# Kernel tuning notes

Measured on AMD Instinct MI355X. Metric: run time of the kernel, lower is better.

Reference implementation:

```python
import jax, jax.numpy as jnp
import numpy as np

EPS = 1e-5

def hard_sigmoid(x):
    return jnp.clip(0.2 * x + 0.5, 0.0, 1.0)

def ln(x, g, b):
    m = jnp.mean(x, axis=-1, keepdims=True)
    std = jnp.sqrt(jnp.var(x, axis=-1, keepdims=True) + EPS)
    return g * ((x - m) / (std + EPS)) + b

def setup_inputs() -> dict:
    key = jax.random.key(0)
    k0, k1, k2 = jax.random.split(key, 3)
    B, T, I, H = 128, 128, 512, 512
    D = I + H
    x = jax.random.normal(k0, (B, T, I), dtype=jnp.float32)
    mask = jnp.ones((B, T), dtype=jnp.int32)
    W = jax.random.normal(k1, (D, H + 1), dtype=jnp.float32) * 0.02
    U = jax.random.normal(k2, (D, H + 1), dtype=jnp.float32) * 0.02
    b = jnp.zeros((H + 1,), dtype=jnp.float32)
    gammas = jnp.ones((2, H + 1), dtype=jnp.float32)
    betas = jnp.zeros((2, H + 1), dtype=jnp.float32)
    return {"x": x, "mask": mask, "W": W, "U": U, "b": b,
            "gammas": gammas, "betas": betas,
            "bucket_size": 128, "depth": 4, "input_dim": 512}

def reference(x, mask, W, U, b, gammas, betas, bucket_size, depth, input_dim):
    B, T, I = x.shape
    H = W.shape[1] - 1
    D = I + H
    # pad input to (input_dim | hidden_dim) layout, time-major, truncate to bucket
    xp = jnp.concatenate([x, jnp.zeros((B, T, H), x.dtype)], axis=-1)
    xs = jnp.transpose(xp, (1, 0, 2))[:bucket_size]          # (Tb, B, D)
    m = (mask.T[:bucket_size] > 0)                            # (Tb, B) bool
    first = jnp.zeros((1, B), dtype=bool)
    shift = jnp.concatenate([m[1:], first], axis=0)
    m2 = m & (~shift)
    m2 = jnp.concatenate([first, m2[:-1]], axis=0)            # (Tb, B)
    Tb = xs.shape[0]
    g0, g1 = gammas[0], gammas[1]
    b0, b1 = betas[0], betas[1]

    def hstep(carry, inp):
        h_tm1, fk_tm1, hv_tm1 = carry
        x_t, fkp_tm1, fkp, mk, mk2, hvp = inp
        sum2 = ln(h_tm1 @ U, g1, b1)                          # (B, H+1)
        s = ln(x_t @ W, g0, b0) + sum2 + b                    # (B, H+1)
        fk_both = hard_sigmoid(s[:, 0])
        fk_t1 = hard_sigmoid(sum2[:, 0] + b[0])
        fk = fkp_tm1 + (1 - fkp_tm1) * (fk_tm1 * fk_both + (1 - fk_tm1) * fk_t1)
        fk = jnp.where(mk2, 0.0, fk)
        h_core = jnp.tanh(s[:, 1:])                           # (B, H)
        h_new = jnp.concatenate([jnp.zeros((B, I), x_t.dtype), h_core], axis=-1)
        h_only = hv_tm1 * fk * (fkp + (1 - fkp) * (1 - hvp))
        x_only = hvp * (1 - fkp) * (1 - fk + fk * (1 - hv_tm1))
        both = (1 - fkp) * fk * hv_tm1 * hvp
        h = h_only[:, None] * h_tm1 + x_only[:, None] * x_t + both[:, None] * h_new
        hv = 1 - (1 - h_only) * (1 - x_only) * (1 - both)
        h = jnp.where(mk[:, None], h, h_tm1)
        fk = jnp.where(mk, fk, fk_tm1)
        hv = jnp.where(mk, hv, hv_tm1)
        fk = jnp.where(mk2, 0.0, fk)
        return (h, fk, hv), (h, fk, hv)

    def vstep(carry, _):
        xv, fkp_tm1, fkp, hvp = carry
        init = (jnp.zeros((B, D), x.dtype),
                jnp.zeros((B,), x.dtype),
                jnp.zeros((B,), x.dtype))
        _, (h_seq, fk_seq, hv_seq) = jax.lax.scan(hstep, init, (xv, fkp_tm1, fkp, m, m2, hvp))
        shifted = jnp.concatenate([fk_seq[1:], jnp.zeros((1, B), x.dtype)], axis=0)
        return (h_seq, fk_seq, shifted, hv_seq), None

    carry0 = (xs,
              jnp.zeros((Tb, B), x.dtype),
              jnp.zeros((Tb, B), x.dtype),
              jnp.ones((Tb, B), x.dtype))
    (h_final, _, _, _), _ = jax.lax.scan(vstep, carry0, None, length=depth)
    return h_final[-1][:, I:]                                  # (B, H)
```

## Files before the change

kernel.cpp:

```cpp
#include <hip/hip_runtime.h>
#include <cstdint>

#define TT 128
#define BB 128
#define II 512
#define HH 512
#define DD 1024
#define NC 513
#define NPAD 520
#define NT 36
#define EPSL 1e-5f

typedef short    s8v  __attribute__((ext_vector_type(8)));
typedef float    f4v  __attribute__((ext_vector_type(4)));
typedef _Float16 h2v  __attribute__((ext_vector_type(2)));

__device__ __forceinline__ ushort f2bf(float f){
  uint u = __builtin_bit_cast(uint, f);
  uint r = (u + 0x7fffu + ((u >> 16) & 1u)) >> 16;
  return (ushort)r;
}
__device__ __forceinline__ float bf2f(ushort s){
  uint u = ((uint)s) << 16;
  return __builtin_bit_cast(float, u);
}
__device__ __forceinline__ float hsig(float x){
  return fminf(fmaxf(0.2f * x + 0.5f, 0.f), 1.f);
}
__device__ __forceinline__ float ftanh(float x){
  float ax = fminf(fabsf(x), 15.f);
  float e  = __builtin_amdgcn_exp2f(ax * 2.885390082f);
  float r  = (e - 1.f) * __builtin_amdgcn_rcpf(e + 1.f);
  return __builtin_copysignf(r, x);
}
__device__ __forceinline__ float dot2(uint a, uint b, float c){
#if __has_builtin(__builtin_amdgcn_fdot2)
  return __builtin_amdgcn_fdot2(__builtin_bit_cast(h2v, a),
                                __builtin_bit_cast(h2v, b), c, false);
#else
  h2v x = __builtin_bit_cast(h2v, a), y = __builtin_bit_cast(h2v, b);
  return fmaf((float)x[1], (float)y[1], fmaf((float)x[0], (float)y[0], c));
#endif
}

__global__ void prepack_B(const float* __restrict__ src, ushort* __restrict__ dst){
  int idx = blockIdx.x * 256 + threadIdx.x;
  if (idx >= 128 * NT * 16 * 8) return;
  int kl = idx & 7;
  int ni = (idx >> 3) & 15;
  int nt = (idx >> 7) % NT;
  int kc = idx / (NT * 16 * 8);
  int k = kc * 8 + kl;
  int n = nt * 16 + ni;
  float v = (n < NC) ? src[k * NC + n] : 0.f;
  dst[idx] = f2bf(v);
}

__global__ void prepack_Uhi_pk(const float* __restrict__ U, uint* __restrict__ dst,
                               float* __restrict__ ucol){
  int idx = blockIdx.x * 256 + threadIdx.x;
  if (idx < 64 * 512 * 4){
    int j = idx & 3;
    int n = (idx >> 2) & 511;
    int c = idx >> 11;
    int k0 = II + 8 * c + 2 * j;
    _Float16 lo = (_Float16)U[(size_t)k0 * NC + n];
    _Float16 hi = (_Float16)U[(size_t)(k0 + 1) * NC + n];
    dst[idx] = (uint)__builtin_bit_cast(ushort, lo)
             | ((uint)__builtin_bit_cast(ushort, hi) << 16);
  }
  if (idx < 512) ucol[idx] = U[(size_t)(II + idx) * NC + 512];
}

__global__ __launch_bounds__(1024) void gemm_ln(
    const float* __restrict__ A, int amode, int ksteps,
    const ushort* __restrict__ Bpk, ushort* __restrict__ out,
    int do_ln, const float* __restrict__ gam, const float* __restrict__ bet,
    const float* __restrict__ bias)
{
  __shared__ ushort As[64][40];
  __shared__ float red[4][4][16][2];
  int tid = threadIdx.x;
  int lane = tid & 63, wid = tid >> 6;
  int quad = lane >> 4, l16 = lane & 15;
  int wm = wid >> 2, wn = wid & 3;
  int blk = blockIdx.x;

  f4v acc[9];
#pragma unroll
  for (int i = 0; i < 9; i++) acc[i] = (f4v){0.f, 0.f, 0.f, 0.f};

  int arow = tid >> 4;
  int acp  = tid & 15;
  int r = blk * 64 + arow;
  const float* aptr;
  if (amode == 0){ int t = r >> 7, b = r & 127; aptr = A + ((size_t)(b * TT + t)) * II + acp * 2; }
  else           { aptr = A + (size_t)r * DD + acp * 2; }

  for (int ks = 0; ks < ksteps; ks++){
    __syncthreads();
    float2 a2 = *(const float2*)(aptr + ks * 32);
    uint pk = (uint)f2bf(a2.x) | ((uint)f2bf(a2.y) << 16);
    *(uint*)&As[arow][acp * 2] = pk;
    __syncthreads();
    s8v af = *(const s8v*)&As[wm * 16 + l16][quad * 8];
    int kc = ks * 4 + quad;
    const s8v* bp = (const s8v*)Bpk + (size_t)kc * (NT * 16) + l16;
#pragma unroll
    for (int i = 0; i < 9; i++){
      s8v bf = bp[(wn * 9 + i) * 16];
      acc[i] = __builtin_amdgcn_mfma_f32_16x16x32_bf16(af, bf, acc[i], 0, 0, 0);
    }
  }

  int rowbase = blk * 64 + wm * 16 + quad * 4;
  if (do_ln){
    float s1[4], s2[4];
#pragma unroll
    for (int g = 0; g < 4; g++){
      float a = 0.f, q = 0.f;
#pragma unroll
      for (int i = 0; i < 9; i++){ float v = acc[i][g]; a += v; q += v * v; }
#pragma unroll
      for (int m = 1; m < 16; m <<= 1){ a += __shfl_xor(a, m, 64); q += __shfl_xor(q, m, 64); }
      s1[g] = a; s2[g] = q;
    }
    if (l16 == 0){
#pragma unroll
      for (int g = 0; g < 4; g++){
        red[wm][wn][quad * 4 + g][0] = s1[g];
        red[wm][wn][quad * 4 + g][1] = s2[g];
      }
    }
    __syncthreads();
#pragma unroll
    for (int g = 0; g < 4; g++){
      int rr = quad * 4 + g;
      float S1 = red[wm][0][rr][0] + red[wm][1][rr][0] + red[wm][2][rr][0] + red[wm][3][rr][0];
      float S2 = red[wm][0][rr][1] + red[wm][1][rr][1] + red[wm][2][rr][1] + red[wm][3][rr][1];
      float mean = S1 * (1.f / 513.f);
      float var  = S2 * (1.f / 513.f) - mean * mean;
      float inv  = 1.f / (sqrtf(var + EPSL) + EPSL);
      size_t rg = (size_t)(rowbase + g);
#pragma unroll
      for (int i = 0; i < 9; i++){
        int n = wn * 144 + i * 16 + l16;
        if (n < NC){
          float val = gam[n] * ((acc[i][g] - mean) * inv) + bet[n] + bias[n];
          out[rg * NPAD + n] = f2bf(val);
        }
      }
    }
  } else {
#pragma unroll
    for (int g = 0; g < 4; g++){
      size_t rg = (size_t)(rowbase + g);
#pragma unroll
      for (int i = 0; i < 9; i++){
        int n = wn * 144 + i * 16 + l16;
        if (n < NC) out[rg * NPAD + n] = f2bf(acc[i][g]);
      }
    }
  }
}

__global__ __launch_bounds__(1024) void rnn_layer(
    int layer,
    const float* __restrict__ x,
    float* __restrict__ h_seq,
    const ushort* __restrict__ lnXW,
    ushort* __restrict__ vbuf,
    float* __restrict__ fkbuf,
    float* __restrict__ hvbuf,
    const uint* __restrict__ Upk4,
    const float* __restrict__ ucol,
    const int* __restrict__ mask,
    const float* __restrict__ gam1, const float* __restrict__ bet1,
    const float* __restrict__ bias,
    float* __restrict__ out)
{
  __shared__ __align__(16) ushort tanh16[512];
  __shared__ __align__(16) float  tanhvf[512];
  __shared__ __align__(16) float  ypart[512];
  __shared__ float red_a[8], red_q[8], red_p[8];
  __shared__ float sh_v0;
  __shared__ int msk[TT];

  int tid = threadIdx.x;
  const bool lowh = (tid < 512);
  int b = blockIdx.x;
  int lane = tid & 63, wid = tid >> 6;
  const bool lastL = (layer == 3);

  float sv = 0.f;
  float v512 = 0.f;
  float h_lo = 0.f, h_hi = 0.f;
  float fkc = 0.f, hvc = 0.f;
  float g1n = lowh ? gam1[tid] : 0.f;
  float b1n = lowh ? bet1[tid] : 0.f;
  float g10 = gam1[0],  b10 = bet1[0];
  float g1e = gam1[512], b1e = bet1[512];
  float bias0 = bias[0];
  float uc = lowh ? ucol[tid] : 0.f;
  float ho_p = 0.f, xo_p = 0.f, bo_p = 0.f, xu5_p = 0.f;
  int mk_p = 0;

  if (tid < TT) msk[tid] = mask[b * TT + tid];
  if (lowh && lane == 0){ red_a[wid] = 0.f; red_q[wid] = 0.f; red_p[wid] = 0.f; }
  if (tid == 0) sh_v0 = 0.f;
  __syncthreads();

  for (int t = 0; t < TT; t++){
    size_t row = (size_t)(t * BB + b);

    float h_only = 0.f, x_only = 0.f, both = 0.f;
    float xu = 0.f, xlo = 0.f, xhi = 0.f, xu5 = 0.f;
    bool mk = false;
    if (lowh){
      float lw    = bf2f(lnXW[row * NPAD + tid]);
      float lw0   = bf2f(lnXW[row * NPAD]);
      float lw512 = bf2f(lnXW[row * NPAD + 512]);
      xu  = bf2f(vbuf[row * NPAD + tid]);
      xu5 = bf2f(vbuf[row * NPAD + 512]);
      if (layer == 0){ xlo = x[((size_t)(b * TT + t)) * II + tid]; xhi = 0.f; }
      else { xlo = h_seq[row * DD + tid]; xhi = h_seq[row * DD + 512 + tid]; }
      float fkp_tm1 = 0.f, fkp = 0.f, hvp = 1.f;
      if (layer > 0){
        fkp_tm1 = fkbuf[t * BB + b];
        fkp = (t + 1 < TT) ? fkbuf[(t + 1) * BB + b] : 0.f;
        hvp = hvbuf[t * BB + b];
      }
      int mraw  = msk[t];
      int mprev = (t > 0) ? msk[t - 1] : 0;

      if (t > 0){
        float y512 = red_p[0] + red_p[1] + red_p[2] + red_p[3]
                   + red_p[4] + red_p[5] + red_p[6] + red_p[7];
        float nv5 = ho_p * v512 + xo_p * xu5_p + bo_p * y512;
        if (mk_p) v512 = nv5;
        if (tid == 0 && !lastL) vbuf[(row - BB) * NPAD + 512] = f2bf(v512);
      }
      float S = red_a[0] + red_a[1] + red_a[2] + red_a[3]
              + red_a[4] + red_a[5] + red_a[6] + red_a[7];
      float Q = red_q[0] + red_q[1] + red_q[2] + red_q[3]
              + red_q[4] + red_q[5] + red_q[6] + red_q[7];
      S += v512; Q += v512 * v512;
      float v0 = sh_v0;
      float mean = S * (1.f / 513.f);
      float var  = Q * (1.f / 513.f) - mean * mean;
      float inv  = 1.f / (sqrtf(var + EPSL) + EPSL);

      mk = mraw > 0;
      bool mk2 = (t > 0) && (mprev > 0) && !mk;
      float sum20 = (v0 - mean) * inv * g10 + b10;
      float s0 = lw0 + sum20;
      float fk_both = hsig(s0);
      float fk_t1   = hsig(sum20 + bias0);
      float fk = fkp_tm1 + (1.f - fkp_tm1) * (fkc * fk_both + (1.f - fkc) * fk_t1);
      if (mk2) fk = 0.f;
      h_only = hvc * fk * (fkp + (1.f - fkp) * (1.f - hvp));
      x_only = hvp * (1.f - fkp) * (1.f - fk + fk * (1.f - hvc));
      both   = (1.f - fkp) * fk * hvc * hvp;
      float hv = 1.f - (1.f - h_only) * (1.f - x_only) * (1.f - both);
      fkc = mk ? fk : fkc;
      hvc = mk ? hv : hvc;
      if (mk2) fkc = 0.f;

      float sum2 = (sv - mean) * inv * g1n + b1n;
      float s = lw + sum2;
      float th = ftanh(s);
      if (tid == 0){
        float sum2e = (v512 - mean) * inv * g1e + b1e;
        float the = ftanh(lw512 + sum2e);
        tanh16[511] = __builtin_bit_cast(ushort, (_Float16)the);
        tanhvf[511] = the;
      } else {
        tanh16[tid - 1] = __builtin_bit_cast(ushort, (_Float16)th);
        tanhvf[tid - 1] = th;
      }
    }
    __syncthreads();

    float yloc;
    {
      int n = tid & 511;
      int cbase = (tid >> 9) * 32;
      const uint4* up = (const uint4*)Upk4 + (size_t)cbase * 512 + n;
      const uint4* tp = (const uint4*)tanh16 + cbase;
      float y0 = 0.f, y1 = 0.f, y2 = 0.f, y3 = 0.f;
#pragma unroll 8
      for (int c = 0; c < 32; c++){
        uint4 uu = up[(size_t)c * 512];
        uint4 tt = tp[c];
        y0 = dot2(tt.x, uu.x, y0);
        y1 = dot2(tt.y, uu.y, y1);
        y2 = dot2(tt.z, uu.z, y2);
        y3 = dot2(tt.w, uu.w, y3);
      }
      yloc = (y0 + y1) + (y2 + y3);
      if (!lowh) ypart[n] = yloc;
    }
    if (lowh){
      float p = tanhvf[tid] * uc;
#pragma unroll
      for (int m = 1; m < 64; m <<= 1) p += __shfl_xor(p, m, 64);
      if (lane == 0) red_p[wid] = p;
    }
    __syncthreads();

    if (lowh){
      float y = yloc + ypart[tid];
      float nv = h_only * sv + x_only * xu + both * y;
      if (mk) sv = nv;
      float thh = tanhvf[tid];
      float nh_lo = h_only * h_lo + x_only * xlo;
      float nh_hi = h_only * h_hi + x_only * xhi + both * thh;
      if (mk){ h_lo = nh_lo; h_hi = nh_hi; }
      if (!lastL){
        vbuf[row * NPAD + tid] = f2bf(sv);
        h_seq[row * DD + tid] = h_lo;
        h_seq[row * DD + 512 + tid] = h_hi;
        if (tid == 0){ fkbuf[t * BB + b] = fkc; hvbuf[t * BB + b] = hvc; }
      }
      if (lastL && t == TT - 1) out[b * HH + tid] = h_hi;

      ho_p = h_only; xo_p = x_only; bo_p = both; mk_p = mk ? 1 : 0; xu5_p = xu5;

      float a = sv, q = sv * sv;
#pragma unroll
      for (int m = 1; m < 64; m <<= 1){ a += __shfl_xor(a, m, 64); q += __shfl_xor(q, m, 64); }
      if (lane == 0){ red_a[wid] = a; red_q[wid] = q; }
      if (tid == 0) sh_v0 = sv;
    }
    __syncthreads();
  }

  if (tid == 0 && !lastL){
    float y512 = red_p[0] + red_p[1] + red_p[2] + red_p[3]
               + red_p[4] + red_p[5] + red_p[6] + red_p[7];
    float nv5 = ho_p * v512 + xo_p * xu5_p + bo_p * y512;
    if (mk_p) v512 = nv5;
    vbuf[(size_t)((TT - 1) * BB + b) * NPAD + 512] = f2bf(v512);
  }
}

extern "C" void kernel_launch(void* const* d_in, const int* in_sizes, int n_in,
                              void* d_out, int out_size, void* d_ws, size_t ws_size,
                              hipStream_t stream)
{
  (void)in_sizes; (void)n_in; (void)out_size; (void)ws_size;
  const float* x      = (const float*)d_in[0];
  const int*   mask   = (const int*)d_in[1];
  const float* W      = (const float*)d_in[2];
  const float* U      = (const float*)d_in[3];
  const float* bias   = (const float*)d_in[4];
  const float* gammas = (const float*)d_in[5];
  const float* betas  = (const float*)d_in[6];
  float* out = (float*)d_out;

  char* ws = (char*)d_ws;
  size_t off = 0;
  auto alloc = [&](size_t bytes) -> void* {
    void* p = ws + off;
    off += (bytes + 255) & ~(size_t)255;
    return p;
  };
  float*  h_seq = (float*) alloc((size_t)TT * BB * DD * 4);
  ushort* lnXW  = (ushort*)alloc((size_t)TT * BB * NPAD * 2);
  ushort* vbuf  = (ushort*)alloc((size_t)TT * BB * NPAD * 2);
  float*  fkbuf = (float*) alloc((size_t)TT * BB * 4);
  float*  hvbuf = (float*) alloc((size_t)TT * BB * 4);
  ushort* Wpk   = (ushort*)alloc((size_t)128 * NT * 16 * 8 * 2);
  ushort* Upk   = (ushort*)alloc((size_t)128 * NT * 16 * 8 * 2);
  uint*   Upk4  = (uint*)  alloc((size_t)64 * 512 * 4 * 4);
  float*  ucol  = (float*) alloc(512 * 4);

  int npk = 128 * NT * 16 * 8;
  prepack_B<<<dim3((npk + 255) / 256), dim3(256), 0, stream>>>(W, Wpk);
  prepack_B<<<dim3((npk + 255) / 256), dim3(256), 0, stream>>>(U, Upk);
  prepack_Uhi_pk<<<dim3((64 * 512 * 4 + 255) / 256), dim3(256), 0, stream>>>(U, Upk4, ucol);

  const float* g0 = gammas,      *g1 = gammas + NC;
  const float* be0 = betas,      *be1 = betas + NC;

  gemm_ln<<<dim3(256), dim3(1024), 0, stream>>>(x, 0, 16, Wpk, lnXW, 1, g0, be0, bias);
  gemm_ln<<<dim3(256), dim3(1024), 0, stream>>>(x, 0, 16, Upk, vbuf, 0, g0, be0, bias);
  rnn_layer<<<dim3(BB), dim3(1024), 0, stream>>>(0, x, h_seq, lnXW, vbuf, fkbuf, hvbuf,
                                                 Upk4, ucol, mask, g1, be1, bias, out);
  for (int d = 1; d < 4; d++){
    gemm_ln<<<dim3(256), dim3(1024), 0, stream>>>(h_seq, 1, 32, Wpk, lnXW, 1, g0, be0, bias);
    rnn_layer<<<dim3(BB), dim3(1024), 0, stream>>>(d, x, h_seq, lnXW, vbuf, fkbuf, hvbuf,
                                                   Upk4, ucol, mask, g1, be1, bias, out);
  }
}
```

Before: 3.055 ms.

## Cache part of recurrent U weights in LDS and registers across timesteps

The per-step recurrent matvec previously streamed all 32 packed U chunks per thread from global memory every timestep. It now keeps 9 chunks per thread in shared memory (about 144KB) and 8 chunks pinned in registers for the whole sequence, so only 15 chunks per step are still read from global/L2. This cuts repeated weight traffic on the serial critical path. In exchange it raises register pressure at 1024 threads and takes a large share of LDS, and it adds a prologue that loads the cached chunks once per block.

```diff
diff --git a/kernel.cpp b/kernel.cpp
--- a/kernel.cpp
+++ b/kernel.cpp
@@ -163,6 +163,12 @@
     }
   }
 }
+
+#define COREG(r, c) do{ uint4 tt = tp[(c)];                        \
+  y0 = dot2(tt.x, r.x, y0); y1 = dot2(tt.y, r.y, y1);              \
+  y2 = dot2(tt.z, r.z, y2); y3 = dot2(tt.w, r.w, y3); }while(0)
+
+#define PIN4(r) asm volatile("" : "+v"(r.x), "+v"(r.y), "+v"(r.z), "+v"(r.w))
 
 __global__ __launch_bounds__(1024) void rnn_layer(
     int layer,
@@ -179,6 +185,7 @@
     const float* __restrict__ bias,
     float* __restrict__ out)
 {
+  __shared__ __align__(16) uint4  u_lds[18 * 512];
   __shared__ __align__(16) ushort tanh16[512];
   __shared__ __align__(16) float  tanhvf[512];
   __shared__ __align__(16) float  ypart[512];
@@ -205,12 +212,33 @@
   float ho_p = 0.f, xo_p = 0.f, bo_p = 0.f, xu5_p = 0.f;
   int mk_p = 0;
 
+  {
+    const uint4* U4 = (const uint4*)Upk4;
+    for (int i = tid; i < 18 * 512; i += 1024){
+      int slot = i >> 9, n2 = i & 511;
+      int c = (slot < 9) ? slot : 32 + (slot - 9);
+      u_lds[i] = U4[(size_t)c * 512 + n2];
+    }
+  }
+
+  int n_ = tid & 511;
+  int cbase_ = (tid >> 9) * 32;
+  uint4 ur0, ur1, ur2, ur3, ur4, ur5, ur6, ur7;
+  {
+    const uint4* upr = (const uint4*)Upk4 + (size_t)(cbase_ + 9) * 512 + n_;
+    ur0 = upr[0 * 512]; ur1 = upr[1 * 512]; ur2 = upr[2 * 512]; ur3 = upr[3 * 512];
+    ur4 = upr[4 * 512]; ur5 = upr[5 * 512]; ur6 = upr[6 * 512]; ur7 = upr[7 * 512];
+  }
+
   if (tid < TT) msk[tid] = mask[b * TT + tid];
   if (lowh && lane == 0){ red_a[wid] = 0.f; red_q[wid] = 0.f; red_p[wid] = 0.f; }
   if (tid == 0) sh_v0 = 0.f;
   __syncthreads();
 
   for (int t = 0; t < TT; t++){
+    PIN4(ur0); PIN4(ur1); PIN4(ur2); PIN4(ur3);
+    PIN4(ur4); PIN4(ur5); PIN4(ur6); PIN4(ur7);
+
     size_t row = (size_t)(t * BB + b);
 
     float h_only = 0.f, x_only = 0.f, both = 0.f;
@@ -283,22 +311,34 @@
 
     float yloc;
     {
-      int n = tid & 511;
-      int cbase = (tid >> 9) * 32;
-      const uint4* up = (const uint4*)Upk4 + (size_t)cbase * 512 + n;
-      const uint4* tp = (const uint4*)tanh16 + cbase;
+      const uint4* tp = (const uint4*)tanh16;
+      const uint4* ups = (const uint4*)Upk4 + (size_t)(cbase_ + 17) * 512 + n_;
       float y0 = 0.f, y1 = 0.f, y2 = 0.f, y3 = 0.f;
-#pragma unroll 8
-      for (int c = 0; c < 32; c++){
-        uint4 uu = up[(size_t)c * 512];
-        uint4 tt = tp[c];
+#pragma unroll 6
+      for (int c = 0; c < 15; c++){
+        uint4 uu = ups[(size_t)c * 512];
+        uint4 tt = tp[cbase_ + 17 + c];
         y0 = dot2(tt.x, uu.x, y0);
         y1 = dot2(tt.y, uu.y, y1);
         y2 = dot2(tt.z, uu.z, y2);
         y3 = dot2(tt.w, uu.w, y3);
       }
+      COREG(ur0, cbase_ + 9);  COREG(ur1, cbase_ + 10);
+      COREG(ur2, cbase_ + 11); COREG(ur3, cbase_ + 12);
+      COREG(ur4, cbase_ + 13); COREG(ur5, cbase_ + 14);
+      COREG(ur6, cbase_ + 15); COREG(ur7, cbase_ + 16);
+      const uint4* ul = u_lds + (size_t)(tid >> 9) * (9 * 512) + n_;
+#pragma unroll
+      for (int j = 0; j < 9; j++){
+        uint4 uu = ul[j * 512];
+        uint4 tt = tp[cbase_ + j];
+        y0 = dot2(tt.x, uu.x, y0);
+        y1 = dot2(tt.y, uu.y, y1);
+        y2 = dot2(tt.z, uu.z, y2);
+        y3 = dot2(tt.w, uu.w, y3);
+      }
       yloc = (y0 + y1) + (y2 + y3);
-      if (!lowh) ypart[n] = yloc;
+      if (!lowh) ypart[n_] = yloc;
     }
     if (lowh){
       float p = tanhvf[tid] * uc;
```

After: 2.476 ms. 19.0% less time.
